# Performance work log

Hardware: AMD Instinct MI355X
Metric: run time of the kernel (lower is better)

Reference implementation:

```python
import jax, jax.numpy as jnp
import numpy as np

N = 50000      # nodes in batched graph
E = 800000     # directed edges
F_IN = 64      # node_feature_dim
F_E = 16       # edge_feature_dim
H = 4          # heads
C = 64         # hidden_dim per head
HC = H * C     # 256


def setup_inputs() -> dict:
    key = jax.random.key(0)
    ks = jax.random.split(key, 26)
    rn = lambda k, s, scale=0.1: jax.random.normal(k, s, dtype=jnp.float32) * scale
    inp = {}
    inp["x"] = rn(ks[0], (N, F_IN), 1.0)
    inp["edge_src"] = jax.random.randint(ks[1], (E,), 0, N)
    inp["edge_dst"] = jax.random.randint(ks[2], (E,), 0, N)
    inp["edge_attr"] = rn(ks[3], (E, F_E), 1.0)
    # GATConv layer 1 params
    inp["W1"] = rn(ks[4], (F_IN, HC))
    inp["atts1"] = rn(ks[5], (H, C))
    inp["attd1"] = rn(ks[6], (H, C))
    inp["We1"] = rn(ks[7], (F_E, HC))
    inp["atte1"] = rn(ks[8], (H, C))
    inp["b1"] = jnp.zeros((HC,), jnp.float32)
    inp["g1"] = jnp.ones((HC,), jnp.float32)
    inp["be1"] = jnp.zeros((HC,), jnp.float32)
    # GATConv layer 2 params
    inp["W2"] = rn(ks[9], (HC, HC))
    inp["atts2"] = rn(ks[10], (H, C))
    inp["attd2"] = rn(ks[11], (H, C))
    inp["We2"] = rn(ks[12], (F_E, HC))
    inp["atte2"] = rn(ks[13], (H, C))
    inp["b2"] = jnp.zeros((HC,), jnp.float32)
    inp["g2"] = jnp.ones((HC,), jnp.float32)
    inp["be2"] = jnp.zeros((HC,), jnp.float32)
    # output head
    inp["Wout"] = rn(ks[14], (HC, 1))
    inp["bout"] = jnp.zeros((1,), jnp.float32)
    return inp


def _gat_layer(x, src, dst, eattr, W, att_s, att_d, We, att_e, b):
    """PyG GATConv (concat=True, add_self_loops with fill_value='mean', eval so no dropout)."""
    n = x.shape[0]
    e = src.shape[0]
    # self-loop edge attr = mean of incoming edge attrs per node (0 if none)
    deg = jax.ops.segment_sum(jnp.ones((e,), x.dtype), dst, num_segments=n)
    loop_attr = jax.ops.segment_sum(eattr, dst, num_segments=n) / jnp.maximum(deg, 1.0)[:, None]
    loop = jnp.arange(n)
    src2 = jnp.concatenate([src, loop])
    dst2 = jnp.concatenate([dst, loop])
    ea2 = jnp.concatenate([eattr, loop_attr], axis=0)
    xs = (x @ W).reshape(n, H, C)                          # [N,H,C]
    a_s = jnp.einsum('nhc,hc->nh', xs, att_s)              # [N,H]
    a_d = jnp.einsum('nhc,hc->nh', xs, att_d)
    ee = (ea2 @ We).reshape(-1, H, C)                      # [E+N,H,C]
    a_e = jnp.einsum('ehc,hc->eh', ee, att_e)
    logits = jax.nn.leaky_relu(a_s[src2] + a_d[dst2] + a_e, 0.2)  # [E+N,H]
    m = jax.ops.segment_max(logits, dst2, num_segments=n)
    p = jnp.exp(logits - m[dst2])
    denom = jax.ops.segment_sum(p, dst2, num_segments=n)[dst2] + 1e-16
    alpha = p / denom                                      # segment softmax per dst node
    out = jax.ops.segment_sum(xs[src2] * alpha[:, :, None], dst2, num_segments=n)
    return out.reshape(n, HC) + b


def _bn_relu(x, g, b):
    # BatchNorm1d in training mode (batch statistics), eps=1e-5
    mu = x.mean(axis=0)
    var = ((x - mu) ** 2).mean(axis=0)
    return jax.nn.relu(g * (x - mu) * jax.lax.rsqrt(var + 1e-5) + b)


def reference(x, edge_src, edge_dst, edge_attr,
              W1, atts1, attd1, We1, atte1, b1, g1, be1,
              W2, atts2, attd2, We2, atte2, b2, g2, be2,
              Wout, bout):
    h = _gat_layer(x, edge_src, edge_dst, edge_attr, W1, atts1, attd1, We1, atte1, b1)
    h = _bn_relu(h, g1, be1)
    h = _gat_layer(h, edge_src, edge_dst, edge_attr, W2, atts2, attd2, We2, atte2, b2)
    h = _bn_relu(h, g2, be2)
    return h @ Wout + bout
```

## Files before the change

### kernel.cpp

```cpp
#include <hip/hip_runtime.h>
#include <hip/hip_bf16.h>
#include <stdint.h>

#define NNODES 50000
#define NEDGES 800000
#define HC 256

typedef unsigned short u16;
typedef __attribute__((ext_vector_type(8))) short bf16x8;
typedef __attribute__((ext_vector_type(4))) float f32x4;

__device__ __forceinline__ float b2f(u16 v) {
    return __uint_as_float(((unsigned)v) << 16);
}
__device__ __forceinline__ u16 f2b(float f) {
    unsigned u = __float_as_uint(f);
    u += 0x7fff + ((u >> 16) & 1);
    return (u16)(u >> 16);
}

__device__ __constant__ int dPO[19] = {0,16384,16640,16896,20992,21248,21504,21760,22016,
                                       87552,87808,88064,92160,92416,92672,92928,93184,93440,93441};
static const int hPO[19] = {0,16384,16640,16896,20992,21248,21504,21760,22016,
                            87552,87808,88064,92160,92416,92672,92928,93184,93440,93441};
#define TOTP 93441

__global__ void zero_init(unsigned* __restrict__ p, long nwords) {
    long i = (long)blockIdx.x * blockDim.x + threadIdx.x;
    long stride = (long)gridDim.x * blockDim.x;
    for (; i < nwords; i += stride) p[i] = 0u;
}

__global__ void detect_dtype(const unsigned* __restrict__ xbits, int* __restrict__ flag) {
    __shared__ int cnt;
    if (threadIdx.x == 0) cnt = 0;
    __syncthreads();
    int sane = 0;
    for (int i = threadIdx.x; i < 1024; i += 256) {
        unsigned lo = xbits[i] & 0xffffu;
        int e = (int)((lo >> 7) & 0xff);
        if (e >= 117 && e <= 133) sane++;
    }
    atomicAdd(&cnt, sane);
    __syncthreads();
    if (threadIdx.x == 0) *flag = (cnt >= 512) ? 1 : 0;
}

__global__ void cvt_bf16(const void* __restrict__ src, u16* __restrict__ dst, int n,
                         const int* __restrict__ flag) {
    int isbf16 = *flag;
    int i = blockIdx.x * 256 + threadIdx.x;
    int stride = gridDim.x * 256;
    if (isbf16) {
        const u16* s = (const u16*)src;
        for (; i < n; i += stride) dst[i] = s[i];
    } else {
        const float* s = (const float*)src;
        for (; i < n; i += stride) dst[i] = f2b(s[i]);
    }
}

struct Ptrs18 { const void* s[18]; };
__global__ void cvt_params(Ptrs18 p, u16* __restrict__ dst, const int* __restrict__ flag) {
    int i = blockIdx.x * 256 + threadIdx.x;
    if (i >= TOTP) return;
    int isbf16 = *flag;
    int idx = 0;
    #pragma unroll
    for (int j = 1; j < 18; j++) idx += (i >= dPO[j]) ? 1 : 0;
    int rel = i - dPO[idx];
    dst[i] = isbf16 ? ((const u16*)p.s[idx])[rel] : f2b(((const float*)p.s[idx])[rel]);
}

__global__ void proj_weight(const u16* __restrict__ W, const u16* __restrict__ att,
                            float* __restrict__ out, int R) {
    int i = blockIdx.x * 256 + threadIdx.x;
    if (i >= R * 4) return;
    int f = i >> 2, h = i & 3;
    float s = 0.f;
    for (int c = 0; c < 64; c++)
        s += b2f(W[f * 256 + h * 64 + c]) * b2f(att[h * 64 + c]);
    out[i] = s;
}

__global__ void proj_weight2(const u16* __restrict__ W, const u16* __restrict__ atta,
                             const u16* __restrict__ attb,
                             float* __restrict__ outa, float* __restrict__ outb, int R) {
    int i = blockIdx.x * 256 + threadIdx.x;
    if (i >= R * 4) return;
    int f = i >> 2, h = i & 3;
    float sa = 0.f, sb = 0.f;
    for (int c = 0; c < 64; c++) {
        float w = b2f(W[f * 256 + h * 64 + c]);
        sa += w * b2f(atta[h * 64 + c]);
        sb += w * b2f(attb[h * 64 + c]);
    }
    outa[i] = sa;
    outb[i] = sb;
}

__global__ void transpose_w(const u16* __restrict__ W, u16* __restrict__ WT, int K) {
    int i = blockIdx.x * 256 + threadIdx.x;
    if (i >= K * 256) return;
    int k = i / 256, c = i % 256;
    WT[c * K + k] = W[i];
}

__global__ void edge_deg(const int* __restrict__ edst, int* __restrict__ deg) {
    int e = blockIdx.x * 256 + threadIdx.x;
    if (e >= NEDGES) return;
    atomicAdd(&deg[edst[e]], 1);
}

__global__ void block_sum(const int* __restrict__ deg, int* __restrict__ bsums, int n) {
    __shared__ int lds[256];
    int i = blockIdx.x * 256 + threadIdx.x;
    lds[threadIdx.x] = (i < n) ? deg[i] : 0;
    __syncthreads();
    for (int s = 128; s; s >>= 1) {
        if (threadIdx.x < s) lds[threadIdx.x] += lds[threadIdx.x + s];
        __syncthreads();
    }
    if (threadIdx.x == 0) bsums[blockIdx.x] = lds[0];
}

__global__ void scan_bsums(const int* __restrict__ bsums, int* __restrict__ boffs, int nb) {
    __shared__ int lds[256];
    int t = threadIdx.x;
    int v = (t < nb) ? bsums[t] : 0;
    lds[t] = v;
    __syncthreads();
    for (int s = 1; s < 256; s <<= 1) {
        int u = (t >= s) ? lds[t - s] : 0;
        __syncthreads();
        lds[t] += u;
        __syncthreads();
    }
    boffs[t] = lds[t] - v;
}

__global__ void write_offsets(const int* __restrict__ deg, const int* __restrict__ boffs,
                              int* __restrict__ off, int* __restrict__ cursor, int n) {
    __shared__ int lds[256];
    int t = threadIdx.x;
    int i = blockIdx.x * 256 + t;
    int v = (i < n) ? deg[i] : 0;
    lds[t] = v;
    __syncthreads();
    for (int s = 1; s < 256; s <<= 1) {
        int u = (t >= s) ? lds[t - s] : 0;
        __syncthreads();
        lds[t] += u;
        __syncthreads();
    }
    int exc = lds[t] - v + boffs[blockIdx.x];
    if (i < n) { off[i] = exc; cursor[i] = exc; }
}

__global__ __launch_bounds__(256) void edge_stage(
    const void* __restrict__ eattr_raw, const int* __restrict__ flag,
    const int* __restrict__ esrc, const int* __restrict__ edst,
    const float* __restrict__ ve1, const float* __restrict__ ve2,
    int* __restrict__ cursor, uint4* __restrict__ rec) {
    int e = blockIdx.x * 256 + threadIdx.x;
    if (e >= NEDGES) return;
    float a[16];
    if (*flag) {
        const u16* s = (const u16*)eattr_raw + (long)e * 16;
        const uint4* q = (const uint4*)s;
        uint4 q0 = q[0], q1 = q[1];
        unsigned w0[8] = {q0.x, q0.y, q0.z, q0.w, q1.x, q1.y, q1.z, q1.w};
        #pragma unroll
        for (int j = 0; j < 8; j++) {
            a[2 * j] = b2f((u16)(w0[j] & 0xffff));
            a[2 * j + 1] = b2f((u16)(w0[j] >> 16));
        }
    } else {
        const float* s = (const float*)eattr_raw + (long)e * 16;
        #pragma unroll
        for (int j = 0; j < 16; j += 4) {
            float4 q = *(const float4*)(s + j);
            a[j] = q.x; a[j + 1] = q.y; a[j + 2] = q.z; a[j + 3] = q.w;
        }
    }
    float s1[4], s2[4];
    #pragma unroll
    for (int h = 0; h < 4; h++) {
        float t1 = 0.f, t2 = 0.f;
        #pragma unroll
        for (int f = 0; f < 16; f++) {
            t1 += a[f] * ve1[f * 4 + h];
            t2 += a[f] * ve2[f * 4 + h];
        }
        s1[h] = t1;
        s2[h] = t2;
    }
    unsigned a1lo = (unsigned)f2b(s1[0]) | ((unsigned)f2b(s1[1]) << 16);
    unsigned a1hi = (unsigned)f2b(s1[2]) | ((unsigned)f2b(s1[3]) << 16);
    unsigned a2lo = (unsigned)f2b(s2[0]) | ((unsigned)f2b(s2[1]) << 16);
    unsigned a2hi = (unsigned)f2b(s2[2]) | ((unsigned)f2b(s2[3]) << 16);
    int d = edst[e];
    int p = atomicAdd(&cursor[d], 1);
    unsigned src = (unsigned)esrc[e];
    rec[(long)p * 2 + 0] = make_uint4(src, a1lo, a1hi, 0u);
    rec[(long)p * 2 + 1] = make_uint4(src, a2lo, a2hi, 0u);
}

__global__ void bn_coef(const float* __restrict__ stats, const u16* __restrict__ g,
                        const u16* __restrict__ be, float* __restrict__ coef) {
    int c = threadIdx.x;
    float mu = stats[c] * (1.0f / NNODES);
    float var = stats[256 + c] * (1.0f / NNODES) - mu * mu;
    var = fmaxf(var, 0.f);
    float rs = rsqrtf(var + 1e-5f);
    float sc = b2f(g[c]) * rs;
    coef[c] = sc;
    coef[256 + c] = b2f(be[c]) - sc * mu;
}

__global__ __launch_bounds__(256) void bn_apply(u16* __restrict__ h,
                                                const float* __restrict__ coef) {
    long i = (long)blockIdx.x * 256 + threadIdx.x;
    long total = (long)NNODES * (HC / 8);
    long stride = (long)gridDim.x * 256;
    int cpos = (int)(i & 31) * 8;
    float scl[8], shf[8];
    #pragma unroll
    for (int j = 0; j < 8; j++) {
        scl[j] = coef[cpos + j];
        shf[j] = coef[256 + cpos + j];
    }
    for (; i < total; i += stride) {
        uint4 v = *((const uint4*)h + i);
        unsigned w[4] = {v.x, v.y, v.z, v.w};
        #pragma unroll
        for (int q = 0; q < 4; q++) {
            float lo = b2f((u16)(w[q] & 0xffffu));
            float hi = b2f((u16)(w[q] >> 16));
            lo = fmaxf(lo * scl[2 * q] + shf[2 * q], 0.f);
            hi = fmaxf(hi * scl[2 * q + 1] + shf[2 * q + 1], 0.f);
            w[q] = (unsigned)f2b(lo) | ((unsigned)f2b(hi) << 16);
        }
        *((uint4*)h + i) = make_uint4(w[0], w[1], w[2], w[3]);
    }
}

__device__ __forceinline__ void gload_lds16(const u16* g, u16* l) {
    __builtin_amdgcn_global_load_lds(
        (const __attribute__((address_space(1))) unsigned*)g,
        (__attribute__((address_space(3))) unsigned*)l, 16, 0, 0);
}

template <int K>
__global__ __launch_bounds__(256) void gemm_tile(const u16* __restrict__ A,
                                                 const u16* __restrict__ WT,
                                                 u16* __restrict__ out) {
    __shared__ u16 As[128 * 32];
    __shared__ u16 Bs[128 * 32];
    int tid = threadIdx.x;
    int wave = tid >> 6, lane = tid & 63;
    int wr = wave >> 1, wc = wave & 1;
    int quad = lane >> 4, l15 = lane & 15;
    long row0 = (long)(blockIdx.x >> 1) * 128;
    int col0 = (blockIdx.x & 1) * 128;
    int srow = lane >> 2;
    int soct = (lane & 3) * 8;
    f32x4 acc[4][4] = {};
    for (int kk = 0; kk < K; kk += 32) {
        #pragma unroll
        for (int sub = 0; sub < 2; sub++) {
            int rr = wave * 32 + sub * 16;
            long gr = row0 + rr + srow;
            if (gr >= NNODES) gr = NNODES - 1;
            gload_lds16(A + gr * K + kk + soct, &As[rr * 32]);
            gload_lds16(WT + (long)(col0 + rr + srow) * K + kk + soct, &Bs[rr * 32]);
        }
        __syncthreads();
        bf16x8 av[4], bv[4];
        #pragma unroll
        for (int m = 0; m < 4; m++)
            av[m] = *(const bf16x8*)&As[(wr * 64 + m * 16 + l15) * 32 + quad * 8];
        #pragma unroll
        for (int n = 0; n < 4; n++)
            bv[n] = *(const bf16x8*)&Bs[(wc * 64 + n * 16 + l15) * 32 + quad * 8];
        #pragma unroll
        for (int m = 0; m < 4; m++)
            #pragma unroll
            for (int n = 0; n < 4; n++)
                acc[m][n] = __builtin_amdgcn_mfma_f32_16x16x32_bf16(av[m], bv[n],
                                                                    acc[m][n], 0, 0, 0);
        __syncthreads();
    }
    #pragma unroll
    for (int m = 0; m < 4; m++) {
        #pragma unroll
        for (int j = 0; j < 4; j++) {
            long r = row0 + wr * 64 + m * 16 + quad * 4 + j;
            if (r < NNODES) {
                u16* op = out + r * HC + col0 + wc * 64 + l15;
                #pragma unroll
                for (int n = 0; n < 4; n++) op[n * 16] = f2b(acc[m][n][j]);
            }
        }
    }
}

template <int K, bool BN>
__global__ __launch_bounds__(256) void proj_att(const u16* __restrict__ X,
                                                const float* __restrict__ coef,
                                                const float* __restrict__ us,
                                                const float* __restrict__ ud,
                                                float* __restrict__ as_, float* __restrict__ ad_) {
    int wid = (blockIdx.x * 256 + threadIdx.x) >> 6;
    int lane = threadIdx.x & 63;
    if (wid >= NNODES) return;
    float pas[4] = {0.f, 0.f, 0.f, 0.f}, pad[4] = {0.f, 0.f, 0.f, 0.f};
    const u16* row = X + (long)wid * K;
    for (int f = lane; f < K; f += 64) {
        float xv = b2f(row[f]);
        if (BN) xv = fmaxf(xv * coef[f] + coef[256 + f], 0.f);
        #pragma unroll
        for (int h = 0; h < 4; h++) {
            pas[h] += xv * us[f * 4 + h];
            pad[h] += xv * ud[f * 4 + h];
        }
    }
    #pragma unroll
    for (int h = 0; h < 4; h++) {
        for (int o = 32; o; o >>= 1) {
            pas[h] += __shfl_down(pas[h], o);
            pad[h] += __shfl_down(pad[h], o);
        }
    }
    if (lane == 0) {
        #pragma unroll
        for (int h = 0; h < 4; h++) {
            as_[wid * 4 + h] = pas[h];
            ad_[wid * 4 + h] = pad[h];
        }
    }
}

__global__ __launch_bounds__(256) void gat_fused(
    const u16* __restrict__ xs, const float* __restrict__ as_, const float* __restrict__ ad_,
    const uint4* __restrict__ rec, int layer,
    const int* __restrict__ off, const int* __restrict__ deg,
    const u16* __restrict__ bias, u16* __restrict__ out) {
    __shared__ int s_lds[4][64];
    __shared__ float w_lds[4][64][4];
    int wid = (blockIdx.x * 256 + threadIdx.x) >> 6;
    if (wid >= NNODES) return;
    int wave = threadIdx.x >> 6;
    int lane = threadIdx.x & 63;
    int d = wid;
    int st = off[d], dg = deg[d];
    int slot = lane >> 2, h = lane & 3;
    float adv = ad_[d * 4 + h];
    float m = -1e30f, s = 0.f, sae = 0.f;
    const uint4* rbase = rec + (long)st * 2 + layer;

    if (dg <= 64) {
        for (int i = slot; i < dg; i += 16) {
            uint4 r4 = rbase[(long)i * 2];
            int src = (int)r4.x;
            unsigned wsel = (h & 2) ? r4.z : r4.y;
            float aev = b2f((u16)((h & 1) ? (wsel >> 16) : (wsel & 0xffffu)));
            float t = as_[src * 4 + h] + adv + aev;
            float lg = (t > 0.f) ? t : 0.2f * t;
            if (h == 0) s_lds[wave][i] = src;
            w_lds[wave][i][h] = lg;
            sae += aev;
            float mn = fmaxf(m, lg);
            s = s * __expf(m - mn) + __expf(lg - mn);
            m = mn;
        }
        #pragma unroll
        for (int o = 4; o < 64; o <<= 1) {
            float mo = __shfl_xor(m, o), so = __shfl_xor(s, o), ao = __shfl_xor(sae, o);
            float mn = fmaxf(m, mo);
            s = s * __expf(m - mn) + so * __expf(mo - mn);
            m = mn;
            sae += ao;
        }
        float invs, wself;
        {
            float asv = as_[d * 4 + h];
            float l0 = asv + adv + sae / fmaxf((float)dg, 1.f);
            l0 = (l0 > 0.f) ? l0 : 0.2f * l0;
            float mn = fmaxf(m, l0);
            s = s * __expf(m - mn) + __expf(l0 - mn);
            m = mn;
            invs = 1.f / s;
            wself = __expf(l0 - mn) * invs;
        }
        for (int i = slot; i < dg; i += 16)
            w_lds[wave][i][h] = __expf(w_lds[wave][i][h] - m) * invs;

        int cg = lane & 31, half = lane >> 5;
        int ch8 = cg * 8;
        int h2 = cg >> 3;
        float ws2 = __shfl(wself, h2);
        const u16* xbase = xs + ch8;
        float a0, a1, a2, a3, a4, a5, a6, a7;
        {
            uint4 v = *(const uint4*)(xbase + (long)d * HC);
            float wsf = half ? 0.f : ws2;
            a0 = wsf * b2f((u16)(v.x & 0xffffu)); a1 = wsf * b2f((u16)(v.x >> 16));
            a2 = wsf * b2f((u16)(v.y & 0xffffu)); a3 = wsf * b2f((u16)(v.y >> 16));
            a4 = wsf * b2f((u16)(v.z & 0xffffu)); a5 = wsf * b2f((u16)(v.z >> 16));
            a6 = wsf * b2f((u16)(v.w & 0xffffu)); a7 = wsf * b2f((u16)(v.w >> 16));
        }
        int i = half;
        for (; i + 6 < dg; i += 8) {
            float wA = w_lds[wave][i][h2];     int sA = s_lds[wave][i];
            float wB = w_lds[wave][i + 2][h2]; int sB = s_lds[wave][i + 2];
            float wC = w_lds[wave][i + 4][h2]; int sC = s_lds[wave][i + 4];
            float wD = w_lds[wave][i + 6][h2]; int sD = s_lds[wave][i + 6];
            uint4 vA = *(const uint4*)(xbase + (long)sA * HC);
            uint4 vB = *(const uint4*)(xbase + (long)sB * HC);
            uint4 vC = *(const uint4*)(xbase + (long)sC * HC);
            uint4 vD = *(const uint4*)(xbase + (long)sD * HC);
            a0 += wA * b2f((u16)(vA.x & 0xffffu)) + wB * b2f((u16)(vB.x & 0xffffu))
                + wC * b2f((u16)(vC.x & 0xffffu)) + wD * b2f((u16)(vD.x & 0xffffu));
            a1 += wA * b2f((u16)(vA.x >> 16))     + wB * b2f((u16)(vB.x >> 16))
                + wC * b2f((u16)(vC.x >> 16))     + wD * b2f((u16)(vD.x >> 16));
            a2 += wA * b2f((u16)(vA.y & 0xffffu)) + wB * b2f((u16)(vB.y & 0xffffu))
                + wC * b2f((u16)(vC.y & 0xffffu)) + wD * b2f((u16)(vD.y & 0xffffu));
            a3 += wA * b2f((u16)(vA.y >> 16))     + wB * b2f((u16)(vB.y >> 16))
                + wC * b2f((u16)(vC.y >> 16))     + wD * b2f((u16)(vD.y >> 16));
            a4 += wA * b2f((u16)(vA.z & 0xffffu)) + wB * b2f((u16)(vB.z & 0xffffu))
                + wC * b2f((u16)(vC.z & 0xffffu)) + wD * b2f((u16)(vD.z & 0xffffu));
            a5 += wA * b2f((u16)(vA.z >> 16))     + wB * b2f((u16)(vB.z >> 16))
                + wC * b2f((u16)(vC.z >> 16))     + wD * b2f((u16)(vD.z >> 16));
            a6 += wA * b2f((u16)(vA.w & 0xffffu)) + wB * b2f((u16)(vB.w & 0xffffu))
                + wC * b2f((u16)(vC.w & 0xffffu)) + wD * b2f((u16)(vD.w & 0xffffu));
            a7 += wA * b2f((u16)(vA.w >> 16))     + wB * b2f((u16)(vB.w >> 16))
                + wC * b2f((u16)(vC.w >> 16))     + wD * b2f((u16)(vD.w >> 16));
        }
        for (; i < dg; i += 2) {
            float wA = w_lds[wave][i][h2]; int sA = s_lds[wave][i];
            uint4 vA = *(const uint4*)(xbase + (long)sA * HC);
            a0 += wA * b2f((u16)(vA.x & 0xffffu)); a1 += wA * b2f((u16)(vA.x >> 16));
            a2 += wA * b2f((u16)(vA.y & 0xffffu)); a3 += wA * b2f((u16)(vA.y >> 16));
            a4 += wA * b2f((u16)(vA.z & 0xffffu)); a5 += wA * b2f((u16)(vA.z >> 16));
            a6 += wA * b2f((u16)(vA.w & 0xffffu)); a7 += wA * b2f((u16)(vA.w >> 16));
        }
        a0 += __shfl_xor(a0, 32); a1 += __shfl_xor(a1, 32);
        a2 += __shfl_xor(a2, 32); a3 += __shfl_xor(a3, 32);
        a4 += __shfl_xor(a4, 32); a5 += __shfl_xor(a5, 32);
        a6 += __shfl_xor(a6, 32); a7 += __shfl_xor(a7, 32);
        if (half == 0) {
            uint4 bv = *(const uint4*)(bias + ch8);
            a0 += b2f((u16)(bv.x & 0xffffu)); a1 += b2f((u16)(bv.x >> 16));
            a2 += b2f((u16)(bv.y & 0xffffu)); a3 += b2f((u16)(bv.y >> 16));
            a4 += b2f((u16)(bv.z & 0xffffu)); a5 += b2f((u16)(bv.z >> 16));
            a6 += b2f((u16)(bv.w & 0xffffu)); a7 += b2f((u16)(bv.w >> 16));
            uint4 ov;
            ov.x = (unsigned)f2b(a0) | ((unsigned)f2b(a1) << 16);
            ov.y = (unsigned)f2b(a2) | ((unsigned)f2b(a3) << 16);
            ov.z = (unsigned)f2b(a4) | ((unsigned)f2b(a5) << 16);
            ov.w = (unsigned)f2b(a6) | ((unsigned)f2b(a7) << 16);
            *(uint4*)(out + (long)d * HC + ch8) = ov;
        }
        return;
    }

    for (int base = 0; base < dg; base += 16) {
        int i = base + slot;
        float lg = -1e30f, aev = 0.f, w = 0.f;
        if (i < dg) {
            uint4 r4 = rbase[(long)i * 2];
            int src = (int)r4.x;
            unsigned wsel = (h & 2) ? r4.z : r4.y;
            aev = b2f((u16)((h & 1) ? (wsel >> 16) : (wsel & 0xffffu)));
            float t = as_[src * 4 + h] + adv + aev;
            lg = (t > 0.f) ? t : 0.2f * t;
        }
        sae += aev;
        float mn = fmaxf(m, lg);
        if (i < dg) w = __expf(lg - mn);
        s = s * __expf(m - mn) + w;
        m = mn;
    }
    #pragma unroll
    for (int o = 4; o < 64; o <<= 1) {
        float mo = __shfl_xor(m, o), so = __shfl_xor(s, o), ao = __shfl_xor(sae, o);
        float mn = fmaxf(m, mo);
        s = s * __expf(m - mn) + so * __expf(mo - mn);
        m = mn;
        sae += ao;
    }
    float invs, wself;
    {
        float asv = as_[d * 4 + h];
        float l0 = asv + adv + sae / fmaxf((float)dg, 1.f);
        l0 = (l0 > 0.f) ? l0 : 0.2f * l0;
        float mn = fmaxf(m, l0);
        s = s * __expf(m - mn) + __expf(l0 - mn);
        m = mn;
        invs = 1.f / s;
        wself = __expf(l0 - mn) * invs;
    }
    int h2 = lane >> 4;
    float m2 = __shfl(m, h2);
    float is2 = __shfl(invs, h2);
    float ws2 = __shfl(wself, h2);
    float adv2 = __shfl(adv, h2);
    int cb = lane * 4;
    float a0, a1, a2, a3;
    {
        uint2 v = *(const uint2*)(xs + (long)d * HC + cb);
        a0 = ws2 * b2f((u16)(v.x & 0xffffu)); a1 = ws2 * b2f((u16)(v.x >> 16));
        a2 = ws2 * b2f((u16)(v.y & 0xffffu)); a3 = ws2 * b2f((u16)(v.y >> 16));
    }
    int slot16 = lane & 15;
    int lhi = lane & 48;
    for (int base = 0; base < dg; base += 16) {
        int cnt = min(16, dg - base);
        float wv = 0.f;
        int srcl = 0;
        if (slot16 < cnt) {
            uint4 r4 = rbase[(long)(base + slot16) * 2];
            srcl = (int)r4.x;
            unsigned wsel = (h2 & 2) ? r4.z : r4.y;
            float aev = b2f((u16)((h2 & 1) ? (wsel >> 16) : (wsel & 0xffffu)));
            float t = as_[srcl * 4 + h2] + adv2 + aev;
            t = (t > 0.f) ? t : 0.2f * t;
            wv = __expf(t - m2) * is2;
        }
        for (int j = 0; j < cnt; j++) {
            float w0 = __shfl(wv, lhi | j);
            int s0 = __shfl(srcl, j);
            uint2 v0 = *(const uint2*)(xs + (long)s0 * HC + cb);
            a0 += w0 * b2f((u16)(v0.x & 0xffffu));
            a1 += w0 * b2f((u16)(v0.x >> 16));
            a2 += w0 * b2f((u16)(v0.y & 0xffffu));
            a3 += w0 * b2f((u16)(v0.y >> 16));
        }
    }
    u16 o0 = f2b(a0 + b2f(bias[cb + 0]));
    u16 o1 = f2b(a1 + b2f(bias[cb + 1]));
    u16 o2 = f2b(a2 + b2f(bias[cb + 2]));
    u16 o3 = f2b(a3 + b2f(bias[cb + 3]));
    uint2 ov;
    ov.x = (unsigned)o0 | ((unsigned)o1 << 16);
    ov.y = (unsigned)o2 | ((unsigned)o3 << 16);
    *(uint2*)(out + (long)d * HC + cb) = ov;
}

__global__ void bn_stats(const u16* __restrict__ h, float* __restrict__ stats) {
    int c = threadIdx.x;
    float s = 0.f, q = 0.f;
    for (int r = blockIdx.x; r < NNODES; r += gridDim.x) {
        float v = b2f(h[(long)r * HC + c]);
        s += v;
        q += v * v;
    }
    atomicAdd(&stats[c], s);
    atomicAdd(&stats[256 + c], q);
}

__global__ __launch_bounds__(256) void out_head(const u16* __restrict__ h,
                                                const float* __restrict__ coef,
                                                const u16* __restrict__ wout,
                                                const u16* __restrict__ bout,
                                                void* __restrict__ y,
                                                const int* __restrict__ flag) {
    int wid = (blockIdx.x * 256 + threadIdx.x) >> 6;
    int lane = threadIdx.x & 63;
    if (wid >= NNODES) return;
    const u16* r = h + (long)wid * HC + lane * 4;
    int c0 = lane * 4;
    float p = 0.f;
    #pragma unroll
    for (int j = 0; j < 4; j++) {
        float v = b2f(r[j]);
        v = fmaxf(v * coef[c0 + j] + coef[256 + c0 + j], 0.f);
        p += v * b2f(wout[c0 + j]);
    }
    for (int o = 32; o; o >>= 1) p += __shfl_down(p, o);
    if (lane == 0) {
        float v = p + b2f(bout[0]);
        if (*flag) ((u16*)y)[wid] = f2b(v);
        else       ((float*)y)[wid] = v;
    }
}

extern "C" void kernel_launch(void* const* d_in, const int* in_sizes, int n_in,
                              void* d_out, int out_size, void* d_ws, size_t ws_size,
                              hipStream_t stream) {
    (void)in_sizes; (void)n_in; (void)out_size; (void)ws_size;
    const void* x_raw     = d_in[0];
    const int*  esrc      = (const int*)d_in[1];
    const int*  edst      = (const int*)d_in[2];
    const void* eattr_raw = d_in[3];

    char* ws = (char*)d_ws;
    size_t o = 0;
    auto alloc = [&](size_t bytes) -> char* {
        o = (o + 255) & ~(size_t)255;
        char* p = ws + o;
        o += bytes;
        return p;
    };
    int* dflag = (int*)alloc(256);
    u16* xb   = (u16*)alloc((size_t)NNODES * 64 * 2);
    u16* pall = (u16*)alloc((size_t)TOTP * 2);
    u16 *W1b = pall + hPO[0], *atts1b = pall + hPO[1], *attd1b = pall + hPO[2],
        *We1b = pall + hPO[3], *atte1b = pall + hPO[4], *b1b = pall + hPO[5],
        *g1b = pall + hPO[6], *be1b = pall + hPO[7], *W2b = pall + hPO[8],
        *atts2b = pall + hPO[9], *attd2b = pall + hPO[10], *We2b = pall + hPO[11],
        *atte2b = pall + hPO[12], *b2b = pall + hPO[13], *g2b = pall + hPO[14],
        *be2b = pall + hPO[15], *Woutb = pall + hPO[16], *boutb = pall + hPO[17];
    u16* WT1 = (u16*)alloc(256 * 64 * 2);
    u16* WT2 = (u16*)alloc(256 * 256 * 2);
    float* ve1 = (float*)alloc(64 * 4);
    float* ve2 = (float*)alloc(64 * 4);
    float* us1 = (float*)alloc(256 * 4);
    float* ud1 = (float*)alloc(256 * 4);
    float* us2 = (float*)alloc(1024 * 4);
    float* ud2 = (float*)alloc(1024 * 4);
    float* coef1 = (float*)alloc(512 * 4);
    float* coef2 = (float*)alloc(512 * 4);
    int* deg = (int*)alloc((size_t)NNODES * 4);
    float* stats1 = (float*)alloc(512 * 4);
    float* stats2 = (float*)alloc(512 * 4);
    size_t zero_end = o;
    size_t zero_begin = (size_t)((char*)deg - ws);
    int* off = (int*)alloc((size_t)NNODES * 4);
    int* cursor = (int*)alloc((size_t)NNODES * 4);
    int* bsums = (int*)alloc(256 * 4);
    int* boffs = (int*)alloc(256 * 4);
    uint4* rec = (uint4*)alloc((size_t)NEDGES * 32);
    float* as_ = (float*)alloc((size_t)NNODES * 16);
    float* ad_ = (float*)alloc((size_t)NNODES * 16);
    u16* bufA = (u16*)alloc((size_t)NNODES * HC * 2);
    u16* bufB = (u16*)alloc((size_t)NNODES * HC * 2);

    long zwords = (long)((zero_end - zero_begin) / 4);
    zero_init<<<128, 256, 0, stream>>>((unsigned*)(ws + zero_begin), zwords);
    detect_dtype<<<1, 256, 0, stream>>>((const unsigned*)x_raw, dflag);

    cvt_bf16<<<2048, 256, 0, stream>>>(x_raw, xb, NNODES * 64, dflag);
    Ptrs18 pp;
    for (int i = 0; i < 18; i++) pp.s[i] = d_in[4 + i];
    cvt_params<<<(TOTP + 255) / 256, 256, 0, stream>>>(pp, pall, dflag);

    transpose_w<<<64, 256, 0, stream>>>(W1b, WT1, 64);
    transpose_w<<<256, 256, 0, stream>>>(W2b, WT2, 256);
    proj_weight<<<1, 256, 0, stream>>>(We1b, atte1b, ve1, 16);
    proj_weight<<<1, 256, 0, stream>>>(We2b, atte2b, ve2, 16);
    proj_weight2<<<1, 256, 0, stream>>>(W1b, atts1b, attd1b, us1, ud1, 64);
    proj_weight2<<<4, 256, 0, stream>>>(W2b, atts2b, attd2b, us2, ud2, 256);

    int eblocks = (NEDGES + 255) / 256;
    int nb = (NNODES + 255) / 256;
    edge_deg<<<eblocks, 256, 0, stream>>>(edst, deg);
    block_sum<<<nb, 256, 0, stream>>>(deg, bsums, NNODES);
    scan_bsums<<<1, 256, 0, stream>>>(bsums, boffs, nb);
    write_offsets<<<nb, 256, 0, stream>>>(deg, boffs, off, cursor, NNODES);
    edge_stage<<<eblocks, 256, 0, stream>>>(eattr_raw, dflag, esrc, edst, ve1, ve2,
                                            cursor, rec);

    int gtiles = ((NNODES + 127) / 128) * 2;
    int wblocks = (NNODES * 64 + 255) / 256;

    gemm_tile<64><<<gtiles, 256, 0, stream>>>(xb, WT1, bufA);
    proj_att<64, false><<<wblocks, 256, 0, stream>>>(xb, nullptr, us1, ud1, as_, ad_);
    gat_fused<<<wblocks, 256, 0, stream>>>(bufA, as_, ad_, rec, 0, off, deg, b1b, bufB);
    bn_stats<<<512, 256, 0, stream>>>(bufB, stats1);
    bn_coef<<<1, 256, 0, stream>>>(stats1, g1b, be1b, coef1);

    bn_apply<<<2048, 256, 0, stream>>>(bufB, coef1);
    gemm_tile<256><<<gtiles, 256, 0, stream>>>(bufB, WT2, bufA);
    proj_att<256, false><<<wblocks, 256, 0, stream>>>(bufB, nullptr, us2, ud2, as_, ad_);
    gat_fused<<<wblocks, 256, 0, stream>>>(bufA, as_, ad_, rec, 1, off, deg, b2b, bufB);
    bn_stats<<<512, 256, 0, stream>>>(bufB, stats2);
    bn_coef<<<1, 256, 0, stream>>>(stats2, g2b, be2b, coef2);

    out_head<<<wblocks, 256, 0, stream>>>(bufB, coef2, Woutb, boutb, d_out, dflag);
}
```

Before: 562.7 us.

## Split GAT aggregation into attention pass and column-sliced gather kernel

Replaces the fused per-node attention-plus-aggregation kernel with two kernels. The first computes softmax weights per edge and head, writing them to a head-major buffer plus self-loop weights. The second gathers source features in 32-column slices, one slice per block, so concurrently running blocks touch a narrower band of the feature matrix and may reuse L2 better. Edge records are also split into per-layer arrays with a separate source index array. The cost is an extra launch and extra global traffic for the attention weights, and each slice re-reads the edge indices and weights eight times.

```diff
diff --git a/kernel.cpp b/kernel.cpp
--- a/kernel.cpp
+++ b/kernel.cpp
@@ -161,7 +161,8 @@
     const void* __restrict__ eattr_raw, const int* __restrict__ flag,
     const int* __restrict__ esrc, const int* __restrict__ edst,
     const float* __restrict__ ve1, const float* __restrict__ ve2,
-    int* __restrict__ cursor, uint4* __restrict__ rec) {
+    int* __restrict__ cursor, uint4* __restrict__ rec1, uint4* __restrict__ rec2,
+    int* __restrict__ src_csr) {
     int e = blockIdx.x * 256 + threadIdx.x;
     if (e >= NEDGES) return;
     float a[16];
@@ -202,8 +203,9 @@
     int d = edst[e];
     int p = atomicAdd(&cursor[d], 1);
     unsigned src = (unsigned)esrc[e];
-    rec[(long)p * 2 + 0] = make_uint4(src, a1lo, a1hi, 0u);
-    rec[(long)p * 2 + 1] = make_uint4(src, a2lo, a2hi, 0u);
+    rec1[p] = make_uint4(src, a1lo, a1hi, 0u);
+    rec2[p] = make_uint4(src, a2lo, a2hi, 0u);
+    src_csr[p] = (int)src;
 }
 
 __global__ void bn_coef(const float* __restrict__ stats, const u16* __restrict__ g,
@@ -341,12 +343,11 @@
     }
 }
 
-__global__ __launch_bounds__(256) void gat_fused(
-    const u16* __restrict__ xs, const float* __restrict__ as_, const float* __restrict__ ad_,
-    const uint4* __restrict__ rec, int layer,
+__global__ __launch_bounds__(256) void gat_attn(
+    const float* __restrict__ as_, const float* __restrict__ ad_,
+    const uint4* __restrict__ recl,
     const int* __restrict__ off, const int* __restrict__ deg,
-    const u16* __restrict__ bias, u16* __restrict__ out) {
-    __shared__ int s_lds[4][64];
+    float* __restrict__ af, float* __restrict__ wselfp) {
     __shared__ float w_lds[4][64][4];
     int wid = (blockIdx.x * 256 + threadIdx.x) >> 6;
     if (wid >= NNODES) return;
@@ -357,17 +358,16 @@
     int slot = lane >> 2, h = lane & 3;
     float adv = ad_[d * 4 + h];
     float m = -1e30f, s = 0.f, sae = 0.f;
-    const uint4* rbase = rec + (long)st * 2 + layer;
+    const uint4* rbase = recl + st;
 
     if (dg <= 64) {
         for (int i = slot; i < dg; i += 16) {
-            uint4 r4 = rbase[(long)i * 2];
+            uint4 r4 = rbase[i];
             int src = (int)r4.x;
             unsigned wsel = (h & 2) ? r4.z : r4.y;
             float aev = b2f((u16)((h & 1) ? (wsel >> 16) : (wsel & 0xffffu)));
             float t = as_[src * 4 + h] + adv + aev;
             float lg = (t > 0.f) ? t : 0.2f * t;
-            if (h == 0) s_lds[wave][i] = src;
             w_lds[wave][i][h] = lg;
             sae += aev;
             float mn = fmaxf(m, lg);
@@ -393,75 +393,9 @@
             invs = 1.f / s;
             wself = __expf(l0 - mn) * invs;
         }
+        if (slot == 0) wselfp[d * 4 + h] = wself;
         for (int i = slot; i < dg; i += 16)
-            w_lds[wave][i][h] = __expf(w_lds[wave][i][h] - m) * invs;
-
-        int cg = lane & 31, half = lane >> 5;
-        int ch8 = cg * 8;
-        int h2 = cg >> 3;
-        float ws2 = __shfl(wself, h2);
-        const u16* xbase = xs + ch8;
-        float a0, a1, a2, a3, a4, a5, a6, a7;
-        {
-            uint4 v = *(const uint4*)(xbase + (long)d * HC);
-            float wsf = half ? 0.f : ws2;
-            a0 = wsf * b2f((u16)(v.x & 0xffffu)); a1 = wsf * b2f((u16)(v.x >> 16));
-            a2 = wsf * b2f((u16)(v.y & 0xffffu)); a3 = wsf * b2f((u16)(v.y >> 16));
-            a4 = wsf * b2f((u16)(v.z & 0xffffu)); a5 = wsf * b2f((u16)(v.z >> 16));
-            a6 = wsf * b2f((u16)(v.w & 0xffffu)); a7 = wsf * b2f((u16)(v.w >> 16));
-        }
-        int i = half;
-        for (; i + 6 < dg; i += 8) {
-            float wA = w_lds[wave][i][h2];     int sA = s_lds[wave][i];
-            float wB = w_lds[wave][i + 2][h2]; int sB = s_lds[wave][i + 2];
-            float wC = w_lds[wave][i + 4][h2]; int sC = s_lds[wave][i + 4];
-            float wD = w_lds[wave][i + 6][h2]; int sD = s_lds[wave][i + 6];
-            uint4 vA = *(const uint4*)(xbase + (long)sA * HC);
-            uint4 vB = *(const uint4*)(xbase + (long)sB * HC);
-            uint4 vC = *(const uint4*)(xbase + (long)sC * HC);
-            uint4 vD = *(const uint4*)(xbase + (long)sD * HC);
-            a0 += wA * b2f((u16)(vA.x & 0xffffu)) + wB * b2f((u16)(vB.x & 0xffffu))
-                + wC * b2f((u16)(vC.x & 0xffffu)) + wD * b2f((u16)(vD.x & 0xffffu));
-            a1 += wA * b2f((u16)(vA.x >> 16))     + wB * b2f((u16)(vB.x >> 16))
-                + wC * b2f((u16)(vC.x >> 16))     + wD * b2f((u16)(vD.x >> 16));
-            a2 += wA * b2f((u16)(vA.y & 0xffffu)) + wB * b2f((u16)(vB.y & 0xffffu))
-                + wC * b2f((u16)(vC.y & 0xffffu)) + wD * b2f((u16)(vD.y & 0xffffu));
-            a3 += wA * b2f((u16)(vA.y >> 16))     + wB * b2f((u16)(vB.y >> 16))
-                + wC * b2f((u16)(vC.y >> 16))     + wD * b2f((u16)(vD.y >> 16));
-            a4 += wA * b2f((u16)(vA.z & 0xffffu)) + wB * b2f((u16)(vB.z & 0xffffu))
-                + wC * b2f((u16)(vC.z & 0xffffu)) + wD * b2f((u16)(vD.z & 0xffffu));
-            a5 += wA * b2f((u16)(vA.z >> 16))     + wB * b2f((u16)(vB.z >> 16))
-                + wC * b2f((u16)(vC.z >> 16))     + wD * b2f((u16)(vD.z >> 16));
-            a6 += wA * b2f((u16)(vA.w & 0xffffu)) + wB * b2f((u16)(vB.w & 0xffffu))
-                + wC * b2f((u16)(vC.w & 0xffffu)) + wD * b2f((u16)(vD.w & 0xffffu));
-            a7 += wA * b2f((u16)(vA.w >> 16))     + wB * b2f((u16)(vB.w >> 16))
-                + wC * b2f((u16)(vC.w >> 16))     + wD * b2f((u16)(vD.w >> 16));
-        }
-        for (; i < dg; i += 2) {
-            float wA = w_lds[wave][i][h2]; int sA = s_lds[wave][i];
-            uint4 vA = *(const uint4*)(xbase + (long)sA * HC);
-            a0 += wA * b2f((u16)(vA.x & 0xffffu)); a1 += wA * b2f((u16)(vA.x >> 16));
-            a2 += wA * b2f((u16)(vA.y & 0xffffu)); a3 += wA * b2f((u16)(vA.y >> 16));
-            a4 += wA * b2f((u16)(vA.z & 0xffffu)); a5 += wA * b2f((u16)(vA.z >> 16));
-            a6 += wA * b2f((u16)(vA.w & 0xffffu)); a7 += wA * b2f((u16)(vA.w >> 16));
-        }
-        a0 += __shfl_xor(a0, 32); a1 += __shfl_xor(a1, 32);
-        a2 += __shfl_xor(a2, 32); a3 += __shfl_xor(a3, 32);
-        a4 += __shfl_xor(a4, 32); a5 += __shfl_xor(a5, 32);
-        a6 += __shfl_xor(a6, 32); a7 += __shfl_xor(a7, 32);
-        if (half == 0) {
-            uint4 bv = *(const uint4*)(bias + ch8);
-            a0 += b2f((u16)(bv.x & 0xffffu)); a1 += b2f((u16)(bv.x >> 16));
-            a2 += b2f((u16)(bv.y & 0xffffu)); a3 += b2f((u16)(bv.y >> 16));
-            a4 += b2f((u16)(bv.z & 0xffffu)); a5 += b2f((u16)(bv.z >> 16));
-            a6 += b2f((u16)(bv.w & 0xffffu)); a7 += b2f((u16)(bv.w >> 16));
-            uint4 ov;
-            ov.x = (unsigned)f2b(a0) | ((unsigned)f2b(a1) << 16);
-            ov.y = (unsigned)f2b(a2) | ((unsigned)f2b(a3) << 16);
-            ov.z = (unsigned)f2b(a4) | ((unsigned)f2b(a5) << 16);
-            ov.w = (unsigned)f2b(a6) | ((unsigned)f2b(a7) << 16);
-            *(uint4*)(out + (long)d * HC + ch8) = ov;
-        }
+            af[h * NEDGES + st + i] = __expf(w_lds[wave][i][h] - m) * invs;
         return;
     }
 
@@ -469,7 +403,7 @@
         int i = base + slot;
         float lg = -1e30f, aev = 0.f, w = 0.f;
         if (i < dg) {
-            uint4 r4 = rbase[(long)i * 2];
+            uint4 r4 = rbase[i];
             int src = (int)r4.x;
             unsigned wsel = (h & 2) ? r4.z : r4.y;
             aev = b2f((u16)((h & 1) ? (wsel >> 16) : (wsel & 0xffffu)));
@@ -501,51 +435,71 @@
         invs = 1.f / s;
         wself = __expf(l0 - mn) * invs;
     }
-    int h2 = lane >> 4;
-    float m2 = __shfl(m, h2);
-    float is2 = __shfl(invs, h2);
-    float ws2 = __shfl(wself, h2);
-    float adv2 = __shfl(adv, h2);
-    int cb = lane * 4;
-    float a0, a1, a2, a3;
+    if (slot == 0) wselfp[d * 4 + h] = wself;
+    for (int i = slot; i < dg; i += 16) {
+        uint4 r4 = rbase[i];
+        int src = (int)r4.x;
+        unsigned wsel = (h & 2) ? r4.z : r4.y;
+        float aev = b2f((u16)((h & 1) ? (wsel >> 16) : (wsel & 0xffffu)));
+        float t = as_[src * 4 + h] + adv + aev;
+        t = (t > 0.f) ? t : 0.2f * t;
+        af[h * NEDGES + st + i] = __expf(t - m) * invs;
+    }
+}
+
+__global__ __launch_bounds__(256) void gat_gather(
+    const u16* __restrict__ xs, const float* __restrict__ af,
+    const float* __restrict__ wselfp, const int* __restrict__ src_csr,
+    const int* __restrict__ off, const int* __restrict__ deg,
+    const u16* __restrict__ bias, u16* __restrict__ out) {
+    int b = blockIdx.x;
+    int slice = b & 7;
+    int dgrp = b >> 3;
+    int wave = threadIdx.x >> 6, lane = threadIdx.x & 63;
+    int d = dgrp * 4 + wave;
+    int g = lane >> 4, l15 = lane & 15;
+    int hd = slice >> 1;
+    int c0 = slice * 32 + l15 * 2;
+    int st = off[d], dg = deg[d];
+    const float* afh = af + (long)hd * NEDGES + st;
+    const int* sc = src_csr + st;
+    const u16* xcol = xs + c0;
+    float a0, a1;
     {
-        uint2 v = *(const uint2*)(xs + (long)d * HC + cb);
-        a0 = ws2 * b2f((u16)(v.x & 0xffffu)); a1 = ws2 * b2f((u16)(v.x >> 16));
-        a2 = ws2 * b2f((u16)(v.y & 0xffffu)); a3 = ws2 * b2f((u16)(v.y >> 16));
-    }
-    int slot16 = lane & 15;
-    int lhi = lane & 48;
-    for (int base = 0; base < dg; base += 16) {
-        int cnt = min(16, dg - base);
-        float wv = 0.f;
-        int srcl = 0;
-        if (slot16 < cnt) {
-            uint4 r4 = rbase[(long)(base + slot16) * 2];
-            srcl = (int)r4.x;
-            unsigned wsel = (h2 & 2) ? r4.z : r4.y;
-            float aev = b2f((u16)((h2 & 1) ? (wsel >> 16) : (wsel & 0xffffu)));
-            float t = as_[srcl * 4 + h2] + adv2 + aev;
-            t = (t > 0.f) ? t : 0.2f * t;
-            wv = __expf(t - m2) * is2;
-        }
-        for (int j = 0; j < cnt; j++) {
-            float w0 = __shfl(wv, lhi | j);
-            int s0 = __shfl(srcl, j);
-            uint2 v0 = *(const uint2*)(xs + (long)s0 * HC + cb);
-            a0 += w0 * b2f((u16)(v0.x & 0xffffu));
-            a1 += w0 * b2f((u16)(v0.x >> 16));
-            a2 += w0 * b2f((u16)(v0.y & 0xffffu));
-            a3 += w0 * b2f((u16)(v0.y >> 16));
-        }
-    }
-    u16 o0 = f2b(a0 + b2f(bias[cb + 0]));
-    u16 o1 = f2b(a1 + b2f(bias[cb + 1]));
-    u16 o2 = f2b(a2 + b2f(bias[cb + 2]));
-    u16 o3 = f2b(a3 + b2f(bias[cb + 3]));
-    uint2 ov;
-    ov.x = (unsigned)o0 | ((unsigned)o1 << 16);
-    ov.y = (unsigned)o2 | ((unsigned)o3 << 16);
-    *(uint2*)(out + (long)d * HC + cb) = ov;
+        float wsf = (g == 0) ? wselfp[d * 4 + hd] : 0.f;
+        unsigned v = *(const unsigned*)(xcol + (long)d * HC);
+        a0 = wsf * b2f((u16)(v & 0xffffu));
+        a1 = wsf * b2f((u16)(v >> 16));
+    }
+    int i = g;
+    for (; i + 12 < dg; i += 16) {
+        int s0 = sc[i], s1 = sc[i + 4], s2 = sc[i + 8], s3 = sc[i + 12];
+        float w0 = afh[i], w1 = afh[i + 4], w2 = afh[i + 8], w3 = afh[i + 12];
+        unsigned v0 = *(const unsigned*)(xcol + (long)s0 * HC);
+        unsigned v1 = *(const unsigned*)(xcol + (long)s1 * HC);
+        unsigned v2 = *(const unsigned*)(xcol + (long)s2 * HC);
+        unsigned v3 = *(const unsigned*)(xcol + (long)s3 * HC);
+        a0 += w0 * b2f((u16)(v0 & 0xffffu)) + w1 * b2f((u16)(v1 & 0xffffu))
+            + w2 * b2f((u16)(v2 & 0xffffu)) + w3 * b2f((u16)(v3 & 0xffffu));
+        a1 += w0 * b2f((u16)(v0 >> 16)) + w1 * b2f((u16)(v1 >> 16))
+            + w2 * b2f((u16)(v2 >> 16)) + w3 * b2f((u16)(v3 >> 16));
+    }
+    for (; i < dg; i += 4) {
+        int s0 = sc[i];
+        float w0 = afh[i];
+        unsigned v0 = *(const unsigned*)(xcol + (long)s0 * HC);
+        a0 += w0 * b2f((u16)(v0 & 0xffffu));
+        a1 += w0 * b2f((u16)(v0 >> 16));
+    }
+    a0 += __shfl_xor(a0, 16); a1 += __shfl_xor(a1, 16);
+    a0 += __shfl_xor(a0, 32); a1 += __shfl_xor(a1, 32);
+    if (g == 0) {
+        unsigned bv = *(const unsigned*)(bias + c0);
+        a0 += b2f((u16)(bv & 0xffffu));
+        a1 += b2f((u16)(bv >> 16));
+        unsigned ov = (unsigned)f2b(a0) | ((unsigned)f2b(a1) << 16);
+        *(unsigned*)(out + (long)d * HC + c0) = ov;
+    }
 }
 
 __global__ void bn_stats(const u16* __restrict__ h, float* __restrict__ stats) {
@@ -631,7 +585,11 @@
     int* cursor = (int*)alloc((size_t)NNODES * 4);
     int* bsums = (int*)alloc(256 * 4);
     int* boffs = (int*)alloc(256 * 4);
-    uint4* rec = (uint4*)alloc((size_t)NEDGES * 32);
+    uint4* rec1 = (uint4*)alloc((size_t)NEDGES * 16);
+    uint4* rec2 = (uint4*)alloc((size_t)NEDGES * 16);
+    int* src_csr = (int*)alloc((size_t)NEDGES * 4);
+    float* af = (float*)alloc((size_t)4 * NEDGES * 4);
+    float* wselfp = (float*)alloc((size_t)NNODES * 16);
     float* as_ = (float*)alloc((size_t)NNODES * 16);
     float* ad_ = (float*)alloc((size_t)NNODES * 16);
     u16* bufA = (u16*)alloc((size_t)NNODES * HC * 2);
@@ -660,21 +618,24 @@
     scan_bsums<<<1, 256, 0, stream>>>(bsums, boffs, nb);
     write_offsets<<<nb, 256, 0, stream>>>(deg, boffs, off, cursor, NNODES);
     edge_stage<<<eblocks, 256, 0, stream>>>(eattr_raw, dflag, esrc, edst, ve1, ve2,
-                                            cursor, rec);
+                                            cursor, rec1, rec2, src_csr);
 
     int gtiles = ((NNODES + 127) / 128) * 2;
     int wblocks = (NNODES * 64 + 255) / 256;
+    int gblocks = (NNODES / 4) * 8;
 
     gemm_tile<64><<<gtiles, 256, 0, stream>>>(xb, WT1, bufA);
     proj_att<64, false><<<wblocks, 256, 0, stream>>>(xb, nullptr, us1, ud1, as_, ad_);
-    gat_fused<<<wblocks, 256, 0, stream>>>(bufA, as_, ad_, rec, 0, off, deg, b1b, bufB);
+    gat_attn<<<wblocks, 256, 0, stream>>>(as_, ad_, rec1, off, deg, af, wselfp);
+    gat_gather<<<gblocks, 256, 0, stream>>>(bufA, af, wselfp, src_csr, off, deg, b1b, bufB);
     bn_stats<<<512, 256, 0, stream>>>(bufB, stats1);
     bn_coef<<<1, 256, 0, stream>>>(stats1, g1b, be1b, coef1);
 
     bn_apply<<<2048, 256, 0, stream>>>(bufB, coef1);
     gemm_tile<256><<<gtiles, 256, 0, stream>>>(bufB, WT2, bufA);
     proj_att<256, false><<<wblocks, 256, 0, stream>>>(bufB, nullptr, us2, ud2, as_, ad_);
-    gat_fused<<<wblocks, 256, 0, stream>>>(bufA, as_, ad_, rec, 1, off, deg, b2b, bufB);
+    gat_attn<<<wblocks, 256, 0, stream>>>(as_, ad_, rec2, off, deg, af, wselfp);
+    gat_gather<<<gblocks, 256, 0, stream>>>(bufA, af, wselfp, src_csr, off, deg, b2b, bufB);
     bn_stats<<<512, 256, 0, stream>>>(bufB, stats2);
     bn_coef<<<1, 256, 0, stream>>>(stats2, g2b, be2b, coef2);
 
```

After: 806.5 us. 1.43x slower.
